# Performance work log

Measured on AMD Instinct MI355X. Metric: run time of the kernel, lower is better.

The kernel has to match this reference:

```python
import jax, jax.numpy as jnp
import numpy as np

HID = 768
INNER = 1536   # hidden_size * expand_factor
NSTATE = 16
KCONV = 4
EPS = 1e-5


def _layernorm(x, w, b):
    mu = jnp.mean(x, axis=-1, keepdims=True)
    var = jnp.mean(jnp.square(x - mu), axis=-1, keepdims=True)
    return (x - mu) * jax.lax.rsqrt(var + EPS) * w + b


def setup_inputs() -> dict:
    key = jax.random.key(0)
    ks = jax.random.split(key, 8)
    B, S = 2, 2048
    s_in = 1.0 / np.sqrt(HID).astype(np.float32)
    s_inner = 1.0 / np.sqrt(INNER).astype(np.float32)
    s_k = 1.0 / np.sqrt(KCONV).astype(np.float32)
    return {
        "x": jax.random.normal(ks[0], (B, S, HID), jnp.float32),
        "norm_w": jnp.ones((HID,), jnp.float32),
        "norm_b": jnp.zeros((HID,), jnp.float32),
        "W_in": jax.random.normal(ks[1], (HID, 2 * INNER), jnp.float32) * s_in,
        "conv_w": jax.random.normal(ks[2], (INNER, 1, KCONV), jnp.float32) * s_k,  # OIH depthwise
        "W_xproj": jax.random.normal(ks[3], (INNER, 2 * NSTATE + INNER), jnp.float32) * s_inner,
        "A_log": jax.random.normal(ks[4], (NSTATE,), jnp.float32),
        "D": jnp.ones((INNER,), jnp.float32),
        "W_ssm_out": jax.random.normal(ks[5], (INNER, INNER), jnp.float32) * s_inner,
        "W_out": jax.random.normal(ks[6], (INNER, HID), jnp.float32) * s_inner,
    }


def _selective_ssm(u, W_xproj, A_log, D, W_ssm_out):
    # u: (B, S, INNER)
    proj = u @ W_xproj                                   # (B,S,2N+INNER)
    Bm = proj[..., :NSTATE]                              # (B,S,N)
    Cm = proj[..., NSTATE:2 * NSTATE]                    # (B,S,N)
    delta = jax.nn.softplus(proj[..., 2 * NSTATE:])      # (B,S,INNER)
    A = -jnp.exp(A_log)                                  # (N,)

    def step(h, inp):
        d_t, b_t, c_t, u_t = inp                          # (B,INNER),(B,N),(B,N),(B,INNER)
        dA = jnp.exp(d_t[:, None, :] * A[None, :, None])  # (B,N,INNER)
        h = dA * h + (d_t * u_t)[:, None, :] * b_t[:, :, None]
        y = jnp.einsum('bnh,bn->bh', h, c_t)
        return h, y

    B_, S_, _ = u.shape
    h0 = jnp.zeros((B_, NSTATE, INNER), u.dtype)
    xs = (jnp.moveaxis(delta, 1, 0), jnp.moveaxis(Bm, 1, 0),
          jnp.moveaxis(Cm, 1, 0), jnp.moveaxis(u, 1, 0))
    _, ys = jax.lax.scan(step, h0, xs)                   # (S,B,INNER)
    y = jnp.moveaxis(ys, 0, 1) + D * u
    return y @ W_ssm_out


def reference(x, norm_w, norm_b, W_in, conv_w, W_xproj, A_log, D, W_ssm_out, W_out):
    residual = x
    xn = _layernorm(x, norm_w, norm_b)
    xp = xn @ W_in                                       # (B,S,2*INNER)
    u, gate = jnp.split(xp, 2, axis=-1)
    # causal depthwise conv1d (torch pads k-1 both sides then truncates -> left pad k-1)
    uc = jax.lax.conv_general_dilated(
        jnp.swapaxes(u, 1, 2), conv_w, window_strides=(1,),
        padding=[(KCONV - 1, 0)], dimension_numbers=('NCH', 'OIH', 'NCH'),
        feature_group_count=INNER)
    u = jax.nn.silu(jnp.swapaxes(uc, 1, 2))              # (B,S,INNER)
    y = _selective_ssm(u, W_xproj, A_log, D, W_ssm_out)
    y = y * jax.nn.silu(gate)
    out = y @ W_out + residual                           # dropout is identity in eval
    return out
```

## Files before the change

### kernel.cpp

```cpp
#include <hip/hip_runtime.h>
#include <cstdint>
#include <cmath>

#define HID 768
#define INNER 1536
#define NST 16
#define SEQ 2048
#define BATCH 2
#define MTOK 4096
#define CHUNK 64
#define NCHUNK 32
#define LOG2E 1.44269504088896f

typedef unsigned short u16;
typedef __bf16 bf16x8 __attribute__((ext_vector_type(8)));
typedef float f32x4 __attribute__((ext_vector_type(4)));

__device__ __forceinline__ u16 f2b(float f) {
  union { float f; unsigned u; } a; a.f = f;
  unsigned r = a.u + 0x7FFFu + ((a.u >> 16) & 1u);
  return (u16)(r >> 16);
}

__device__ __forceinline__ float b2f(u16 h) {
  union { unsigned u; float f; } a; a.u = ((unsigned)h) << 16;
  return a.f;
}

__device__ __forceinline__ void gl2lds16(const u16* g, u16* l) {
  __builtin_amdgcn_global_load_lds(
      (const __attribute__((address_space(1))) void*)g,
      (__attribute__((address_space(3))) void*)l, 16, 0, 0);
}

__global__ __launch_bounds__(256)
void prologue(const float* __restrict__ x, const float* __restrict__ nw,
              const float* __restrict__ nb, u16* __restrict__ xn,
              const float* __restrict__ W0, u16* __restrict__ T0,
              const float* __restrict__ W1, u16* __restrict__ T1,
              const float* __restrict__ W2, u16* __restrict__ T2,
              const float* __restrict__ W3, u16* __restrict__ T3) {
  __shared__ float tb[32][33];
  __shared__ float r1[4], r2[4];
  const int tid = threadIdx.x;
  int bid = blockIdx.x;

  if (bid < MTOK) {
    const float* xr = x + (long)bid * HID;
    float v0 = xr[tid], v1 = xr[tid + 256], v2 = xr[tid + 512];
    float s1 = v0 + v1 + v2;
    float s2 = v0 * v0 + v1 * v1 + v2 * v2;
#pragma unroll
    for (int o = 32; o > 0; o >>= 1) { s1 += __shfl_down(s1, o); s2 += __shfl_down(s2, o); }
    if ((tid & 63) == 0) { r1[tid >> 6] = s1; r2[tid >> 6] = s2; }
    __syncthreads();
    s1 = r1[0] + r1[1] + r1[2] + r1[3];
    s2 = r2[0] + r2[1] + r2[2] + r2[3];
    const float mu = s1 * (1.f / HID);
    float var = s2 * (1.f / HID) - mu * mu;
    const float rs = rsqrtf(var + 1e-5f);
    xn[(long)bid * HID + tid]       = f2b((v0 - mu) * rs * nw[tid]       + nb[tid]);
    xn[(long)bid * HID + tid + 256] = f2b((v1 - mu) * rs * nw[tid + 256] + nb[tid + 256]);
    xn[(long)bid * HID + tid + 512] = f2b((v2 - mu) * rs * nw[tid + 512] + nb[tid + 512]);
    return;
  }

  bid -= MTOK;
  const float* W; u16* Wt; int K, N, nbx;
  if (bid < 2304)       {              W = W0; Wt = T0; K = 768;  N = 3072; nbx = 96; }
  else if (bid < 4800)  { bid -= 2304; W = W1; Wt = T1; K = 1536; N = 1568; nbx = 52; }
  else if (bid < 7104)  { bid -= 4800; W = W2; Wt = T2; K = 1536; N = 1536; nbx = 48; }
  else                  { bid -= 7104; W = W3; Wt = T3; K = 1536; N = 768;  nbx = 24; }
  const int tx = tid & 31, ty = tid >> 5;
  const int n0 = (bid % nbx) * 32, k0 = (bid / nbx) * 32;
#pragma unroll
  for (int r = 0; r < 4; ++r) {
    int kk = k0 + ty + r * 8;
    int nn = n0 + tx;
    tb[ty + r * 8][tx] = (nn < N) ? W[(long)kk * N + nn] : 0.f;
  }
  __syncthreads();
#pragma unroll
  for (int r = 0; r < 4; ++r) {
    int nn = n0 + ty + r * 8;
    int kk = k0 + tx;
    Wt[(long)nn * K + kk] = f2b(tb[tx][ty + r * 8]);
  }
}

template <int BM, int BN, int EPI>
__global__ __launch_bounds__(256)
void gemm_bt(const u16* __restrict__ A, const u16* __restrict__ Bt,
             float* __restrict__ C0, float* __restrict__ C1, float* __restrict__ C2,
             u16* __restrict__ Cb, const float* __restrict__ E0,
             const u16* __restrict__ Eb, int K, int Nstore) {
  constexpr int WTM = BM / 2;
  constexpr int WTN = BN / 2;
  constexpr int FI = WTM / 16;
  constexpr int FJ = WTN / 16;
  __shared__ u16 As[BM * 32];
  __shared__ u16 Bs[BN * 32];
  const int tid = threadIdx.x;
  const int lane = tid & 63;
  const int wave = tid >> 6;
  const int wm = wave >> 1, wn = wave & 1;
  const int l16 = lane & 15, l4 = lane >> 4;
  const long bm = (long)blockIdx.y * BM;
  const long bn = (long)blockIdx.x * BN;

  f32x4 acc[FI][FJ] = {};

  const int r0 = tid >> 2;
  const int kg = (tid & 3) * 8;

  for (int k0 = 0; k0 < K; k0 += 32) {
#pragma unroll
    for (int q = 0; q < BM / 64; ++q)
      gl2lds16(A + (bm + r0 + q * 64) * K + kg + k0, As + ((q * 256 + tid) * 8));
#pragma unroll
    for (int q = 0; q < BN / 64; ++q)
      gl2lds16(Bt + (bn + r0 + q * 64) * K + kg + k0, Bs + ((q * 256 + tid) * 8));
    __syncthreads();
    bf16x8 af[FI], bfr[FJ];
#pragma unroll
    for (int i = 0; i < FI; ++i)
      af[i] = *(const bf16x8*)&As[(wm * WTM + i * 16 + l16) * 32 + l4 * 8];
#pragma unroll
    for (int j = 0; j < FJ; ++j)
      bfr[j] = *(const bf16x8*)&Bs[(wn * WTN + j * 16 + l16) * 32 + l4 * 8];
#pragma unroll
    for (int i = 0; i < FI; ++i)
#pragma unroll
      for (int j = 0; j < FJ; ++j)
        acc[i][j] = __builtin_amdgcn_mfma_f32_16x16x32_bf16(af[i], bfr[j], acc[i][j], 0, 0, 0);
    __syncthreads();
  }

#pragma unroll
  for (int i = 0; i < FI; ++i) {
    const long rr = bm + wm * WTM + i * 16 + l4 * 4;
#pragma unroll
    for (int j = 0; j < FJ; ++j) {
      const int cc = (int)bn + wn * WTN + j * 16 + l16;
#pragma unroll
      for (int r = 0; r < 4; ++r) {
        const long row = rr + r;
        const float v = acc[i][j][r];
        if (EPI == 0) {
          if (cc < INNER) C0[row * INNER + cc] = v;
          else            Cb[row * INNER + (cc - INNER)] = f2b(v);
        } else if (EPI == 1) {
          if (cc < 16) C0[row * 16 + cc] = v;
          else if (cc < 32) C1[row * 16 + (cc - 16)] = v;
          else if (cc < Nstore) {
            float sp = (v > 20.f) ? v : log1pf(__expf(v));
            C2[row * 1536 + (cc - 32)] = sp;
          }
        } else if (EPI == 2) {
          float g = b2f(Eb[row * INNER + cc]);
          float s = g / (1.f + __expf(-g));
          Cb[row * INNER + cc] = f2b(v * s);
        } else {
          C0[row * 768 + cc] = v + E0[row * 768 + cc];
        }
      }
    }
  }
}

__global__ __launch_bounds__(256)
void conv_silu(const float* __restrict__ xu, const float* __restrict__ cw,
               float* __restrict__ uf, u16* __restrict__ ub) {
  const int c = blockIdx.x * 256 + threadIdx.x;
  const long m = blockIdx.y;
  const int t = (int)(m & (SEQ - 1));
  const float w0 = cw[c * 4 + 0], w1 = cw[c * 4 + 1], w2 = cw[c * 4 + 2], w3 = cw[c * 4 + 3];
  float acc = w3 * xu[m * 1536 + c];
  if (t >= 1) acc += w2 * xu[(m - 1) * 1536 + c];
  if (t >= 2) acc += w1 * xu[(m - 2) * 1536 + c];
  if (t >= 3) acc += w0 * xu[(m - 3) * 1536 + c];
  const float s = acc / (1.f + __expf(-acc));
  uf[m * 1536 + c] = s;
  ub[m * 1536 + c] = f2b(s);
}

__global__ __launch_bounds__(256)
void scan_phaseA(const float* __restrict__ dlt, const float* __restrict__ uf,
                 const float* __restrict__ Bm, const float* __restrict__ A_log,
                 float* __restrict__ P, float* __restrict__ Q) {
  const int tid = threadIdx.x;
  const int cl = tid >> 2;
  const int sg = tid & 3;
  const int c = blockIdx.x * 64 + cl;
  const int b = blockIdx.y;
  const int ch = blockIdx.z;
  float a2[4];
#pragma unroll
  for (int j = 0; j < 4; ++j) a2[j] = -__expf(A_log[sg * 4 + j]) * LOG2E;
  float h[4] = {0.f, 0.f, 0.f, 0.f};
  float sumd = 0.f;
  const long base = (long)b * SEQ + (long)ch * CHUNK;
  for (int t = 0; t < CHUNK; ++t) {
    const long m = base + t;
    const float d = dlt[m * 1536 + c];
    const float du = d * uf[m * 1536 + c];
    sumd += d;
    const f32x4 Bv = *(const f32x4*)&Bm[m * 16 + sg * 4];
#pragma unroll
    for (int j = 0; j < 4; ++j) {
      const float e = exp2f(a2[j] * d);
      h[j] = e * h[j] + du * Bv[j];
    }
  }
  const long sb = (((long)b * NCHUNK + ch) * NST + sg * 4) * 1536 + c;
#pragma unroll
  for (int j = 0; j < 4; ++j) {
    Q[sb + (long)j * 1536] = h[j];
    P[sb + (long)j * 1536] = exp2f(a2[j] * sumd);
  }
}

__global__ __launch_bounds__(256)
void scan_phaseB(float* __restrict__ P, const float* __restrict__ Q) {
  const long g = (long)blockIdx.x * 256 + threadIdx.x;
  const int c = (int)(g % 1536);
  const int n = (int)((g / 1536) % NST);
  const int b = (int)(g / (1536 * NST));
  float h = 0.f;
  for (int ch = 0; ch < NCHUNK; ++ch) {
    const long idx = (((long)b * NCHUNK + ch) * NST + n) * 1536 + c;
    const float p = P[idx];
    const float q = Q[idx];
    P[idx] = h;
    h = p * h + q;
  }
}

__global__ __launch_bounds__(256)
void scan_phaseC(const float* __restrict__ dlt, const float* __restrict__ uf,
                 const float* __restrict__ Bm, const float* __restrict__ Cm,
                 const float* __restrict__ A_log, const float* __restrict__ Dv,
                 const float* __restrict__ hs, u16* __restrict__ ys) {
  const int tid = threadIdx.x;
  const int cl = tid >> 2;
  const int sg = tid & 3;
  const int c = blockIdx.x * 64 + cl;
  const int b = blockIdx.y;
  const int ch = blockIdx.z;
  float a2[4];
#pragma unroll
  for (int j = 0; j < 4; ++j) a2[j] = -__expf(A_log[sg * 4 + j]) * LOG2E;
  float h[4];
  const long sb = (((long)b * NCHUNK + ch) * NST + sg * 4) * 1536 + c;
#pragma unroll
  for (int j = 0; j < 4; ++j) h[j] = hs[sb + (long)j * 1536];
  const float Dc = Dv[c];
  const long base = (long)b * SEQ + (long)ch * CHUNK;
  for (int t = 0; t < CHUNK; ++t) {
    const long m = base + t;
    const float d = dlt[m * 1536 + c];
    const float uu = uf[m * 1536 + c];
    const float du = d * uu;
    const f32x4 Bv = *(const f32x4*)&Bm[m * 16 + sg * 4];
    const f32x4 Cv = *(const f32x4*)&Cm[m * 16 + sg * 4];
    float y = (sg == 0) ? Dc * uu : 0.f;
#pragma unroll
    for (int j = 0; j < 4; ++j) {
      const float e = exp2f(a2[j] * d);
      h[j] = e * h[j] + du * Bv[j];
      y += h[j] * Cv[j];
    }
    y += __shfl_xor(y, 1);
    y += __shfl_xor(y, 2);
    if (sg == 0) ys[m * 1536 + c] = f2b(y);
  }
}

extern "C" void kernel_launch(void* const* d_in, const int* in_sizes, int n_in,
                              void* d_out, int out_size, void* d_ws, size_t ws_size,
                              hipStream_t stream) {
  const float* x     = (const float*)d_in[0];
  const float* nw    = (const float*)d_in[1];
  const float* nb    = (const float*)d_in[2];
  const float* W_in  = (const float*)d_in[3];
  const float* cw    = (const float*)d_in[4];
  const float* W_xp  = (const float*)d_in[5];
  const float* A_log = (const float*)d_in[6];
  const float* Dv    = (const float*)d_in[7];
  const float* W_so  = (const float*)d_in[8];
  const float* W_out = (const float*)d_in[9];
  float* out = (float*)d_out;

  char* w = (char*)d_ws;
  auto alloc = [&](size_t bytes) {
    char* p = w;
    w += (bytes + 255) & ~(size_t)255;
    return p;
  };
  u16*   xn    = (u16*)  alloc((size_t)MTOK * HID * 2);
  u16*   WtIn  = (u16*)  alloc((size_t)3072 * 768 * 2);
  float* xu    = (float*)alloc((size_t)MTOK * 1536 * 4);
  u16*   gb    = (u16*)  alloc((size_t)MTOK * 1536 * 2);
  float* uf    = (float*)alloc((size_t)MTOK * 1536 * 4);
  u16*   ub    = (u16*)  alloc((size_t)MTOK * 1536 * 2);
  u16*   WtXp  = (u16*)  alloc((size_t)1664 * 1536 * 2);
  float* Bmv   = (float*)alloc((size_t)MTOK * 16 * 4);
  float* Cmv   = (float*)alloc((size_t)MTOK * 16 * 4);
  float* dlt   = (float*)alloc((size_t)MTOK * 1536 * 4);
  float* P     = (float*)alloc((size_t)BATCH * NCHUNK * NST * 1536 * 4);
  float* Q     = (float*)alloc((size_t)BATCH * NCHUNK * NST * 1536 * 4);
  u16*   ys    = (u16*)  alloc((size_t)MTOK * 1536 * 2);
  u16*   WtSo  = (u16*)  alloc((size_t)1536 * 1536 * 2);
  u16*   zb    = (u16*)  alloc((size_t)MTOK * 1536 * 2);
  u16*   WtOut = (u16*)  alloc((size_t)768 * 1536 * 2);

  prologue<<<12352, 256, 0, stream>>>(x, nw, nb, xn,
                                      W_in, WtIn, W_xp, WtXp,
                                      W_so, WtSo, W_out, WtOut);

  gemm_bt<128, 128, 0><<<dim3(24, 32), 256, 0, stream>>>(xn, WtIn, xu, nullptr, nullptr, gb, nullptr, nullptr, 768, 3072);
  conv_silu<<<dim3(6, MTOK), 256, 0, stream>>>(xu, cw, uf, ub);
  gemm_bt<128, 64, 1><<<dim3(26, 32), 256, 0, stream>>>(ub, WtXp, Bmv, Cmv, dlt, nullptr, nullptr, nullptr, 1536, 1568);
  scan_phaseA<<<dim3(24, 2, NCHUNK), 256, 0, stream>>>(dlt, uf, Bmv, A_log, P, Q);
  scan_phaseB<<<192, 256, 0, stream>>>(P, Q);
  scan_phaseC<<<dim3(24, 2, NCHUNK), 256, 0, stream>>>(dlt, uf, Bmv, Cmv, A_log, Dv, P, ys);
  gemm_bt<128, 64, 2><<<dim3(24, 32), 256, 0, stream>>>(ys, WtSo, nullptr, nullptr, nullptr, zb, nullptr, gb, 1536, 1536);
  gemm_bt<64, 64, 3><<<dim3(12, 64), 256, 0, stream>>>(zb, WtOut, out, nullptr, nullptr, nullptr, x, nullptr, 1536, 768);
}
```

Before: 394.3 us.

## Double-buffer GEMM LDS staging with XOR swizzle and enlarge GEMM tiles

```diff
diff --git a/kernel.cpp b/kernel.cpp
--- a/kernel.cpp
+++ b/kernel.cpp
@@ -31,6 +31,15 @@
   __builtin_amdgcn_global_load_lds(
       (const __attribute__((address_space(1))) void*)g,
       (__attribute__((address_space(3))) void*)l, 16, 0, 0);
+}
+
+template <int N>
+__device__ __forceinline__ void vmwait() {
+  if constexpr (N == 0)      asm volatile("s_waitcnt vmcnt(0)" ::: "memory");
+  else if constexpr (N == 2) asm volatile("s_waitcnt vmcnt(2)" ::: "memory");
+  else if constexpr (N == 3) asm volatile("s_waitcnt vmcnt(3)" ::: "memory");
+  else if constexpr (N == 4) asm volatile("s_waitcnt vmcnt(4)" ::: "memory");
+  else static_assert(N == 0 || N == 2 || N == 3 || N == 4, "unsupported vmcnt");
 }
 
 __global__ __launch_bounds__(256)
@@ -98,42 +107,57 @@
   constexpr int WTN = BN / 2;
   constexpr int FI = WTM / 16;
   constexpr int FJ = WTN / 16;
-  __shared__ u16 As[BM * 32];
-  __shared__ u16 Bs[BN * 32];
+  constexpr int NLD = BM / 64 + BN / 64;
+  __shared__ u16 As[2][BM * 32];
+  __shared__ u16 Bs[2][BN * 32];
   const int tid = threadIdx.x;
   const int lane = tid & 63;
   const int wave = tid >> 6;
   const int wm = wave >> 1, wn = wave & 1;
   const int l16 = lane & 15, l4 = lane >> 4;
+  const int swz = (l16 >> 1) & 3;
   const long bm = (long)blockIdx.y * BM;
   const long bn = (long)blockIdx.x * BN;
 
   f32x4 acc[FI][FJ] = {};
 
   const int r0 = tid >> 2;
-  const int kg = (tid & 3) * 8;
-
-  for (int k0 = 0; k0 < K; k0 += 32) {
+  const int kg = ((tid & 3) ^ ((r0 >> 1) & 3)) * 8;
+
+  auto stage = [&](int buf, int k0) {
 #pragma unroll
     for (int q = 0; q < BM / 64; ++q)
-      gl2lds16(A + (bm + r0 + q * 64) * K + kg + k0, As + ((q * 256 + tid) * 8));
+      gl2lds16(A + (bm + r0 + q * 64) * K + kg + k0, &As[buf][(q * 256 + tid) * 8]);
 #pragma unroll
     for (int q = 0; q < BN / 64; ++q)
-      gl2lds16(Bt + (bn + r0 + q * 64) * K + kg + k0, Bs + ((q * 256 + tid) * 8));
-    __syncthreads();
+      gl2lds16(Bt + (bn + r0 + q * 64) * K + kg + k0, &Bs[buf][(q * 256 + tid) * 8]);
+  };
+
+  const int NK = K >> 5;
+  stage(0, 0);
+  int cur = 0;
+  for (int t = 0; t < NK; ++t) {
+    if (t + 1 < NK) {
+      stage(cur ^ 1, (t + 1) << 5);
+      vmwait<NLD>();
+    } else {
+      vmwait<0>();
+    }
+    __builtin_amdgcn_s_barrier();
     bf16x8 af[FI], bfr[FJ];
 #pragma unroll
     for (int i = 0; i < FI; ++i)
-      af[i] = *(const bf16x8*)&As[(wm * WTM + i * 16 + l16) * 32 + l4 * 8];
+      af[i] = *(const bf16x8*)&As[cur][(wm * WTM + i * 16 + l16) * 32 + (l4 ^ swz) * 8];
 #pragma unroll
     for (int j = 0; j < FJ; ++j)
-      bfr[j] = *(const bf16x8*)&Bs[(wn * WTN + j * 16 + l16) * 32 + l4 * 8];
+      bfr[j] = *(const bf16x8*)&Bs[cur][(wn * WTN + j * 16 + l16) * 32 + (l4 ^ swz) * 8];
 #pragma unroll
     for (int i = 0; i < FI; ++i)
 #pragma unroll
       for (int j = 0; j < FJ; ++j)
         acc[i][j] = __builtin_amdgcn_mfma_f32_16x16x32_bf16(af[i], bfr[j], acc[i][j], 0, 0, 0);
-    __syncthreads();
+    __builtin_amdgcn_s_barrier();
+    cur ^= 1;
   }
 
 #pragma unroll
@@ -320,10 +344,10 @@
 
   gemm_bt<128, 128, 0><<<dim3(24, 32), 256, 0, stream>>>(xn, WtIn, xu, nullptr, nullptr, gb, nullptr, nullptr, 768, 3072);
   conv_silu<<<dim3(6, MTOK), 256, 0, stream>>>(xu, cw, uf, ub);
-  gemm_bt<128, 64, 1><<<dim3(26, 32), 256, 0, stream>>>(ub, WtXp, Bmv, Cmv, dlt, nullptr, nullptr, nullptr, 1536, 1568);
+  gemm_bt<128, 128, 1><<<dim3(13, 32), 256, 0, stream>>>(ub, WtXp, Bmv, Cmv, dlt, nullptr, nullptr, nullptr, 1536, 1568);
   scan_phaseA<<<dim3(24, 2, NCHUNK), 256, 0, stream>>>(dlt, uf, Bmv, A_log, P, Q);
   scan_phaseB<<<192, 256, 0, stream>>>(P, Q);
   scan_phaseC<<<dim3(24, 2, NCHUNK), 256, 0, stream>>>(dlt, uf, Bmv, Cmv, A_log, Dv, P, ys);
-  gemm_bt<128, 64, 2><<<dim3(24, 32), 256, 0, stream>>>(ys, WtSo, nullptr, nullptr, nullptr, zb, nullptr, gb, 1536, 1536);
-  gemm_bt<64, 64, 3><<<dim3(12, 64), 256, 0, stream>>>(zb, WtOut, out, nullptr, nullptr, nullptr, x, nullptr, 1536, 768);
-}
+  gemm_bt<128, 128, 2><<<dim3(12, 32), 256, 0, stream>>>(ys, WtSo, nullptr, nullptr, nullptr, zb, nullptr, gb, 1536, 1536);
+  gemm_bt<128, 64, 3><<<dim3(12, 32), 256, 0, stream>>>(zb, WtOut, out, nullptr, nullptr, nullptr, x, nullptr, 1536, 768);
+}
```

Result: no change. 390.4 us (-1.0%).
